# Optimization experiments

Hardware: AMD Instinct MI355X
Metric: run time of the kernel (lower is better)

Reference implementation:

```python
import jax, jax.numpy as jnp
import numpy as np

N_NODES = 50000
N_EDGES = 600000
N_DISCRETE = 70
NH = N_DISCRETE - 6          # 64
EMB = 128                    # n_embedding
D = NH + EMB                 # 192, resdnn/cross input dim
RES_HID = 512                # l_hidden entries
N_RES = 2                    # len(l_hidden)
N_CROSS = 2
PRED_HID = (2 * NH + 512) // 2  # 320
NEG_SLOPE = 0.01


def setup_inputs() -> dict:
    key = jax.random.key(0)
    ks = jax.random.split(key, 24)
    def w(k, shape, fan_in):
        return (jax.random.normal(k, shape, jnp.float32) / np.sqrt(fan_in)).astype(jnp.float32)
    inp = {
        "discrete_x": jax.random.randint(ks[0], (N_NODES, N_DISCRETE), 0, 100, jnp.int64),
        "edge_index": jax.random.randint(ks[1], (2, N_EDGES), 0, N_NODES, jnp.int64),
        # graph embedding linear + 2 GCN layers
        "w_g0": w(ks[2], (NH, EMB), NH), "b_g0": jnp.zeros((EMB,), jnp.float32),
        "w_gcn1": w(ks[3], (EMB, EMB), EMB), "b_gcn1": jnp.zeros((EMB,), jnp.float32),
        "w_gcn2": w(ks[4], (EMB, EMB), EMB), "b_gcn2": jnp.zeros((EMB,), jnp.float32),
        # ResDNN: N_RES dim-preserving residual bottleneck blocks D->RES_HID->D
        "res_w1": w(ks[5], (N_RES, D, RES_HID), D), "res_b1": jnp.zeros((N_RES, RES_HID), jnp.float32),
        "res_w2": w(ks[6], (N_RES, RES_HID, D), RES_HID), "res_b2": jnp.zeros((N_RES, D), jnp.float32),
        # CrossNet: N_CROSS layers
        "cross_w": w(ks[7], (N_CROSS, D), D), "cross_b": jnp.zeros((N_CROSS, D), jnp.float32),
        # Prediction MLP: 2D -> PRED_HID -> 1, sigmoid
        "p_w1": w(ks[8], (2 * D, PRED_HID), 2 * D), "p_b1": jnp.zeros((PRED_HID,), jnp.float32),
        "p_w2": w(ks[9], (PRED_HID, 1), PRED_HID), "p_b2": jnp.zeros((1,), jnp.float32),
    }
    return inp


def _leaky(x):
    return jax.nn.leaky_relu(x, NEG_SLOPE)


def _gcn_conv(x, W, b, row, col, n):
    # PyG GCNConv: linear, then sym-normalized aggregation over A + I, then bias
    h = x @ W
    deg = jax.ops.segment_sum(jnp.ones(row.shape, x.dtype), col, num_segments=n) + 1.0
    dinv = jax.lax.rsqrt(deg)
    norm = dinv[row] * dinv[col]            # [E]
    msg = h[row] * norm[:, None]            # [E, EMB]  (largest intermediate)
    agg = jax.ops.segment_sum(msg, col, num_segments=n)
    agg = agg + h * (dinv * dinv)[:, None]  # self-loop contribution
    return agg + b


def reference(discrete_x, edge_index, w_g0, b_g0, w_gcn1, b_gcn1, w_gcn2, b_gcn2,
              res_w1, res_b1, res_w2, res_b2, cross_w, cross_b,
              p_w1, p_b1, p_w2, p_b2):
    n = discrete_x.shape[0]
    row, col = edge_index[0], edge_index[1]
    # DiscreteFeatureEmbeddingLayer: map n_discrete_features int cols -> nh float dims
    x_d = discrete_x[:, :NH].astype(jnp.float32)
    # graph branch
    x_g = _leaky(x_d @ w_g0 + b_g0)
    x_g = _leaky(_gcn_conv(x_g, w_gcn1, b_gcn1, row, col, n))
    x_g = _leaky(_gcn_conv(x_g, w_gcn2, b_gcn2, row, col, n))
    x = jnp.concatenate([x_d, x_g], axis=-1)  # [N, D]
    # ResDNN: residual bottleneck blocks
    x_deep = x
    for i in range(N_RES):
        h = _leaky(x_deep @ res_w1[i] + res_b1[i])
        x_deep = _leaky(x_deep + h @ res_w2[i] + res_b2[i])
    # CrossNet (DCN): x_{l+1} = x0 * (x_l . w_l) + b_l + x_l
    x0 = x
    x_cross = x
    for i in range(N_CROSS):
        xw = x_cross @ cross_w[i]            # [N]
        x_cross = x0 * xw[:, None] + cross_b[i] + x_cross
    z = jnp.concatenate([x_deep, x_cross], axis=-1)  # [N, 2D]
    h = _leaky(z @ p_w1 + p_b1)
    y = jax.nn.sigmoid(h @ p_w2 + p_b2)
    return y.squeeze(-1)
```

## Files before the change

kernel.cpp:

```cpp
#include <hip/hip_runtime.h>
#include <math.h>

constexpr int NCOLS   = 70;
constexpr int NH      = 64;
constexpr int EMB     = 128;
constexpr int DD      = 192;
constexpr int RES_HID = 512;
constexpr int PRED_HID= 320;

typedef _Float16 f16x8 __attribute__((ext_vector_type(8)));
typedef float    f32x4 __attribute__((ext_vector_type(4)));
#define MFMA16F(a,b,c) __builtin_amdgcn_mfma_f32_16x16x32_f16((a),(b),(c),0,0,0)

constexpr float LO_SCALE   = 4096.0f;
constexpr float LO_DESCALE = 1.0f/4096.0f;
constexpr float Z_SCALE    = 0.0625f;
constexpr float Z_DESCALE  = 16.0f;

__device__ __forceinline__ float leaky(float x){ return x > 0.f ? x : 0.01f*x; }

__global__ void k_hist(const int* __restrict__ col, int* __restrict__ cnt, int E){
  int e = blockIdx.x*256 + threadIdx.x;
  if (e < E) atomicAdd(&cnt[col[e]], 1);
}
__global__ void k_scanA(const int* __restrict__ cnt, int* __restrict__ bsum, int n){
  __shared__ int s;
  if (threadIdx.x == 0) s = 0;
  __syncthreads();
  int i = blockIdx.x*256 + threadIdx.x;
  int v = (i < n) ? cnt[i] : 0;
  #pragma unroll
  for (int o=32;o;o>>=1) v += __shfl_xor(v, o, 64);
  if ((threadIdx.x & 63) == 0) atomicAdd(&s, v);
  __syncthreads();
  if (threadIdx.x == 0) bsum[blockIdx.x] = s;
}
__global__ void k_scanB(int* bsum, int nb){
  __shared__ int s[256];
  __shared__ int carry;
  if (threadIdx.x == 0) carry = 0;
  __syncthreads();
  for (int start = 0; start < nb; start += 256){
    int i = start + threadIdx.x;
    int v = (i < nb) ? bsum[i] : 0;
    s[threadIdx.x] = v; __syncthreads();
    for (int o=1;o<256;o<<=1){
      int t = (threadIdx.x >= o) ? s[threadIdx.x-o] : 0;
      __syncthreads();
      s[threadIdx.x] += t; __syncthreads();
    }
    if (i < nb) bsum[i] = carry + s[threadIdx.x] - v;
    __syncthreads();
    if (threadIdx.x == 255) carry += s[255];
    __syncthreads();
  }
}
__global__ void k_scanC(const int* __restrict__ cnt, const int* __restrict__ bsum,
                        int* __restrict__ base, int* __restrict__ cursor,
                        float* __restrict__ dinv, int n, int E){
  __shared__ int s[256];
  int i = blockIdx.x*256 + threadIdx.x;
  int v = (i < n) ? cnt[i] : 0;
  s[threadIdx.x] = v; __syncthreads();
  for (int o=1;o<256;o<<=1){
    int t = (threadIdx.x >= o) ? s[threadIdx.x-o] : 0;
    __syncthreads();
    s[threadIdx.x] += t; __syncthreads();
  }
  if (i < n){
    int b = bsum[blockIdx.x] + s[threadIdx.x] - v;
    base[i] = b; cursor[i] = b;
    dinv[i] = rsqrtf((float)(v + 1));
  }
  if (i == n-1) base[n] = E;
}
__global__ void k_fill(const int* __restrict__ row, const int* __restrict__ col,
                       const float* __restrict__ dinv, int* __restrict__ cursor,
                       int2* __restrict__ ebin, int E){
  int e = blockIdx.x*256 + threadIdx.x;
  if (e < E){
    int r = row[e], c = col[e];
    int slot = atomicAdd(&cursor[c], 1);
    ebin[slot] = make_int2(r, __float_as_int(dinv[r]));
  }
}

__device__ __forceinline__ void pack_one(const float* __restrict__ W,
                                         _Float16* __restrict__ Wh, _Float16* __restrict__ Wl,
                                         int K, int N, int local){
  int k = local / N, nn = local - k*N;
  float v = W[local];
  _Float16 h = (_Float16)v;
  float lo = (v - (float)h)*LO_SCALE;
  int kc = k >> 5, r = k & 31;
  int lane = (nn & 15) | ((r >> 3) << 4);
  int j = r & 7;
  size_t dst = ((size_t)((nn >> 4)*(K >> 5) + kc) << 9) + lane*8 + j;
  Wh[dst] = h;
  Wl[dst] = (_Float16)lo;
}
__global__ void k_wprep_all(const float* res_w1, const float* res_w2, const float* p_w1,
                            const float* w_g0, const float* w_gcn1, const float* w_gcn2,
                            _Float16* wt1h, _Float16* wt1l, _Float16* wt2h, _Float16* wt2l,
                            _Float16* wph, _Float16* wpl, _Float16* wg0h, _Float16* wg0l,
                            _Float16* wg1h, _Float16* wg1l, _Float16* wg2h, _Float16* wg2l)
{
  int idx = blockIdx.x*256 + threadIdx.x;
  constexpr int SZ = DD*RES_HID;
  constexpr int PZ = 2*DD*PRED_HID;
  if (idx < SZ)                 pack_one(res_w1,           wt1h,      wt1l,      DD, RES_HID, idx);
  else if (idx < 2*SZ)          pack_one(res_w1 + SZ,      wt1h + SZ, wt1l + SZ, DD, RES_HID, idx - SZ);
  else if (idx < 3*SZ)          pack_one(res_w2,           wt2h,      wt2l,      RES_HID, DD, idx - 2*SZ);
  else if (idx < 4*SZ)          pack_one(res_w2 + SZ,      wt2h + SZ, wt2l + SZ, RES_HID, DD, idx - 3*SZ);
  else if (idx < 4*SZ + PZ)     pack_one(p_w1,             wph,       wpl,       2*DD, PRED_HID, idx - 4*SZ);
  else if (idx < 4*SZ + PZ + NH*EMB)
                                pack_one(w_g0,             wg0h,      wg0l,      NH, EMB, idx - 4*SZ - PZ);
  else if (idx < 4*SZ + PZ + NH*EMB + EMB*EMB)
                                pack_one(w_gcn1,           wg1h,      wg1l,      EMB, EMB, idx - 4*SZ - PZ - NH*EMB);
  else if (idx < 4*SZ + PZ + NH*EMB + 2*EMB*EMB)
                                pack_one(w_gcn2,           wg2h,      wg2l,      EMB, EMB, idx - 4*SZ - PZ - NH*EMB - EMB*EMB);
}

__global__ void k_embed(const int* __restrict__ dx, float* __restrict__ A, int n){
  int idx = blockIdx.x*256 + threadIdx.x;
  if (idx < n*NH){
    int i = idx >> 6, j = idx & 63;
    A[(size_t)i*DD + j] = (float)dx[(size_t)i*NCOLS + j];
  }
}

template<int KC>
__global__ __launch_bounds__(256,3)
void k_lin_mfma2(const float* __restrict__ X, int ldx,
                 const _Float16* __restrict__ Wh, const _Float16* __restrict__ Wl,
                 const float* __restrict__ bias,
                 float* __restrict__ out, int ldo, int ooff, int n, int act)
{
  constexpr int K  = KC*32;
  constexpr int KS = K + 4;
  __shared__ __align__(16) _Float16 xh[32*KS];
  __shared__ __align__(16) _Float16 xl[32*KS];
  int i0 = blockIdx.x*32;
  for (int idx = threadIdx.x; idx < 32*K; idx += 256){
    int t = idx / K, k = idx - t*K;
    int i = i0 + t;
    float v = (i < n) ? X[(size_t)i*ldx + k] : 0.f;
    _Float16 h = (_Float16)v;
    xh[t*KS + k] = h;
    xl[t*KS + k] = (_Float16)((v - (float)h)*LO_SCALE);
  }
  __syncthreads();
  int wv = threadIdx.x >> 6, ln = threadIdx.x & 63;
  int cn = ln & 15, kg = ln >> 4;
  f16x8 A0h[KC], A0l[KC], A1h[KC], A1l[KC];
  #pragma unroll
  for (int kc=0;kc<KC;kc++){
    int k0 = kc*32 + kg*8;
    A0h[kc] = *(const f16x8*)&xh[cn*KS + k0];
    A0l[kc] = *(const f16x8*)&xl[cn*KS + k0];
    A1h[kc] = *(const f16x8*)&xh[(16+cn)*KS + k0];
    A1l[kc] = *(const f16x8*)&xl[(16+cn)*KS + k0];
  }
  #pragma unroll
  for (int t=0;t<2;t++){
    int nt = wv*2 + t, n0 = nt*16;
    const _Float16* wbh = Wh + (((size_t)nt*KC) << 9) + ln*8;
    const _Float16* wbl = Wl + (((size_t)nt*KC) << 9) + ln*8;
    f32x4 acc0={0.f,0.f,0.f,0.f}, accL0={0.f,0.f,0.f,0.f};
    f32x4 acc1={0.f,0.f,0.f,0.f}, accL1={0.f,0.f,0.f,0.f};
    #pragma unroll
    for (int kc=0;kc<KC;kc++){
      f16x8 bh = *(const f16x8*)(wbh + ((size_t)kc<<9));
      f16x8 bl = *(const f16x8*)(wbl + ((size_t)kc<<9));
      acc0  = MFMA16F(A0h[kc], bh, acc0);
      accL0 = MFMA16F(A0l[kc], bh, accL0);
      accL0 = MFMA16F(A0h[kc], bl, accL0);
      acc1  = MFMA16F(A1h[kc], bh, acc1);
      accL1 = MFMA16F(A1l[kc], bh, accL1);
      accL1 = MFMA16F(A1h[kc], bl, accL1);
    }
    float bb = bias ? bias[n0 + cn] : 0.f;
    #pragma unroll
    for (int r=0;r<4;r++){
      int ia = i0 + kg*4 + r, ib = ia + 16;
      float v0 = acc0[r] + accL0[r]*LO_DESCALE + bb;
      float v1 = acc1[r] + accL1[r]*LO_DESCALE + bb;
      if (act){ v0 = leaky(v0); v1 = leaky(v1); }
      if (ia < n) out[(size_t)ia*ldo + ooff + n0 + cn] = v0;
      if (ib < n) out[(size_t)ib*ldo + ooff + n0 + cn] = v1;
    }
  }
}

__global__ void k_gather(const float* __restrict__ h, const float* __restrict__ dinv,
                         const int* __restrict__ base, const int2* __restrict__ ebin,
                         const float* __restrict__ bias, float* __restrict__ out,
                         int ldo, int ooff, int n)
{
  int node = blockIdx.x*4 + (threadIdx.x >> 6);
  int lane = threadIdx.x & 63;
  if (node >= n) return;
  int half = lane >> 5, l32 = lane & 31;
  int b0 = base[node], b1 = base[node+1];
  float dc = dinv[node];
  float4 acc = {0.f,0.f,0.f,0.f};
  for (int e = b0 + half; e < b1; e += 2){
    int2 ee = ebin[e];
    float4 hv = ((const float4*)(h + (size_t)ee.x*EMB))[l32];
    float dd = __int_as_float(ee.y);
    acc.x = fmaf(hv.x, dd, acc.x);
    acc.y = fmaf(hv.y, dd, acc.y);
    acc.z = fmaf(hv.z, dd, acc.z);
    acc.w = fmaf(hv.w, dd, acc.w);
  }
  acc.x += __shfl_xor(acc.x, 32, 64);
  acc.y += __shfl_xor(acc.y, 32, 64);
  acc.z += __shfl_xor(acc.z, 32, 64);
  acc.w += __shfl_xor(acc.w, 32, 64);
  float4 hc = ((const float4*)(h + (size_t)node*EMB))[l32];
  float4 bv = ((const float4*)bias)[l32];
  float4 res;
  res.x = leaky((acc.x + hc.x*dc)*dc + bv.x);
  res.y = leaky((acc.y + hc.y*dc)*dc + bv.y);
  res.z = leaky((acc.z + hc.z*dc)*dc + bv.z);
  res.w = leaky((acc.w + hc.w*dc)*dc + bv.w);
  if (half == 0)
    *(float4*)(out + (size_t)node*ldo + ooff + 4*l32) = res;
}

constexpr int XS = 196;
constexpr int HS = 516;

__global__ __launch_bounds__(256,2)
void k_resblock_mfma(const float* __restrict__ X,
                     const _Float16* __restrict__ W1h, const _Float16* __restrict__ W1l,
                     const float* __restrict__ b1,
                     const _Float16* __restrict__ W2h, const _Float16* __restrict__ W2l,
                     const float* __restrict__ b2,
                     float* __restrict__ out, int n)
{
  __shared__ __align__(16) _Float16 xh[32*XS];
  __shared__ __align__(16) _Float16 xl[32*XS];
  __shared__ __align__(16) _Float16 hh[32*HS];
  int i0 = blockIdx.x*32;
  for (int idx = threadIdx.x; idx < 32*DD; idx += 256){
    int t = idx / DD, k = idx - t*DD;
    int i = i0 + t;
    float v = (i < n) ? X[(size_t)i*DD + k] : 0.f;
    _Float16 h = (_Float16)v;
    xh[t*XS + k] = h;
    xl[t*XS + k] = (_Float16)((v - (float)h)*LO_SCALE);
  }
  __syncthreads();
  int wv = threadIdx.x >> 6, ln = threadIdx.x & 63;
  int cn = ln & 15, kg = ln >> 4;

  {
    f16x8 A0h[6], A0l[6], A1h[6], A1l[6];
    #pragma unroll
    for (int kc=0;kc<6;kc++){
      int k0 = kc*32 + kg*8;
      A0h[kc] = *(const f16x8*)&xh[cn*XS + k0];
      A0l[kc] = *(const f16x8*)&xl[cn*XS + k0];
      A1h[kc] = *(const f16x8*)&xh[(16+cn)*XS + k0];
      A1l[kc] = *(const f16x8*)&xl[(16+cn)*XS + k0];
    }
    float bias1[8];
    #pragma unroll
    for (int ct=0;ct<8;ct++) bias1[ct] = b1[(wv*8+ct)*16 + cn];
    const _Float16* pbh = W1h + ((size_t)(wv*8)*6 << 9) + ln*8;
    const _Float16* pbl = W1l + ((size_t)(wv*8)*6 << 9) + ln*8;
    f16x8 Bh[6], Bl[6];
    #pragma unroll
    for (int kc=0;kc<6;kc++){
      Bh[kc] = *(const f16x8*)(pbh + ((size_t)kc<<9));
      Bl[kc] = *(const f16x8*)(pbl + ((size_t)kc<<9));
    }
    #pragma unroll 1
    for (int ct = 0; ct < 8; ct++){
      f16x8 Bh2[6], Bl2[6];
      if (ct < 7){
        const _Float16* nh = pbh + ((size_t)((ct+1)*6) << 9);
        const _Float16* nl = pbl + ((size_t)((ct+1)*6) << 9);
        #pragma unroll
        for (int kc=0;kc<6;kc++){
          Bh2[kc] = *(const f16x8*)(nh + ((size_t)kc<<9));
          Bl2[kc] = *(const f16x8*)(nl + ((size_t)kc<<9));
        }
      }
      f32x4 acc0={0.f,0.f,0.f,0.f}, accL0={0.f,0.f,0.f,0.f};
      f32x4 acc1={0.f,0.f,0.f,0.f}, accL1={0.f,0.f,0.f,0.f};
      #pragma unroll
      for (int kc=0;kc<6;kc++){
        acc0  = MFMA16F(A0h[kc], Bh[kc], acc0);
        accL0 = MFMA16F(A0l[kc], Bh[kc], accL0);
        accL0 = MFMA16F(A0h[kc], Bl[kc], accL0);
        acc1  = MFMA16F(A1h[kc], Bh[kc], acc1);
        accL1 = MFMA16F(A1l[kc], Bh[kc], accL1);
        accL1 = MFMA16F(A1h[kc], Bl[kc], accL1);
      }
      int n0 = (wv*8+ct)*16;
      float bb = bias1[ct];
      #pragma unroll
      for (int r=0;r<4;r++){
        hh[(kg*4+r)*HS + n0 + cn]    = (_Float16)leaky(acc0[r] + accL0[r]*LO_DESCALE + bb);
        hh[(16+kg*4+r)*HS + n0 + cn] = (_Float16)leaky(acc1[r] + accL1[r]*LO_DESCALE + bb);
      }
      #pragma unroll
      for (int kc=0;kc<6;kc++){ Bh[kc]=Bh2[kc]; Bl[kc]=Bl2[kc]; }
    }
  }
  __syncthreads();

  {
    f32x4 acc[3][2], accL[3][2];
    #pragma unroll
    for (int c=0;c<3;c++){
      #pragma unroll
      for (int g=0;g<2;g++){
        acc[c][g]  = (f32x4){0.f,0.f,0.f,0.f};
        accL[c][g] = (f32x4){0.f,0.f,0.f,0.f};
      }
    }
    f16x8 B2h[3], B2l[3];
    #pragma unroll
    for (int c=0;c<3;c++){
      size_t off = ((size_t)((wv*3+c)*16) << 9) + ln*8;
      B2h[c] = *(const f16x8*)(W2h + off);
      B2l[c] = *(const f16x8*)(W2l + off);
    }
    #pragma unroll 1
    for (int kc=0;kc<16;kc++){
      f16x8 N2h[3], N2l[3];
      if (kc < 15){
        #pragma unroll
        for (int c=0;c<3;c++){
          size_t off = ((size_t)((wv*3+c)*16 + kc + 1) << 9) + ln*8;
          N2h[c] = *(const f16x8*)(W2h + off);
          N2l[c] = *(const f16x8*)(W2l + off);
        }
      }
      int k0 = kc*32 + kg*8;
      f16x8 a0 = *(const f16x8*)&hh[cn*HS + k0];
      f16x8 a1 = *(const f16x8*)&hh[(16+cn)*HS + k0];
      #pragma unroll
      for (int c=0;c<3;c++){
        acc[c][0]  = MFMA16F(a0, B2h[c], acc[c][0]);
        accL[c][0] = MFMA16F(a0, B2l[c], accL[c][0]);
        acc[c][1]  = MFMA16F(a1, B2h[c], acc[c][1]);
        accL[c][1] = MFMA16F(a1, B2l[c], accL[c][1]);
      }
      #pragma unroll
      for (int c=0;c<3;c++){ B2h[c]=N2h[c]; B2l[c]=N2l[c]; }
    }
    #pragma unroll
    for (int c=0;c<3;c++){
      int n0 = (wv*3+c)*16;
      float bb = b2[n0 + cn];
      #pragma unroll
      for (int r=0;r<4;r++){
        int m0 = kg*4 + r, m1 = 16 + kg*4 + r;
        float res0 = (float)xh[m0*XS + n0 + cn] + (float)xl[m0*XS + n0 + cn]*LO_DESCALE;
        float res1 = (float)xh[m1*XS + n0 + cn] + (float)xl[m1*XS + n0 + cn]*LO_DESCALE;
        int ia = i0 + m0, ib = i0 + m1;
        if (ia < n) out[(size_t)ia*DD + n0 + cn] = leaky(res0 + acc[c][0][r] + accL[c][0][r]*LO_DESCALE + bb);
        if (ib < n) out[(size_t)ib*DD + n0 + cn] = leaky(res1 + acc[c][1][r] + accL[c][1][r]*LO_DESCALE + bb);
      }
    }
  }
}

constexpr int ZS = 392;

__global__ __launch_bounds__(256,3)
void k_pred_mfma(const float* __restrict__ deep, const float* __restrict__ X0,
                 const float* __restrict__ cw, const float* __restrict__ cb,
                 const _Float16* __restrict__ Wh, const _Float16* __restrict__ Wl,
                 const float* __restrict__ b1,
                 const float* __restrict__ w2, const float* __restrict__ b2,
                 float* __restrict__ y, int n)
{
  __shared__ __align__(16) _Float16 zh[32*ZS];
  __shared__ __align__(16) _Float16 zl[32*ZS];
  __shared__ float sred[4][32];
  int i0 = blockIdx.x*32;
  for (int idx = threadIdx.x; idx < 32*DD; idx += 256){
    int t = idx / DD, k = idx - t*DD;
    int i = i0 + t;
    float v = (i < n) ? deep[(size_t)i*DD + k] : 0.f;
    v *= Z_SCALE;
    _Float16 h = (_Float16)v;
    zh[t*ZS + k] = h;
    zl[t*ZS + k] = (_Float16)((v - (float)h)*LO_SCALE);
  }
  int wv = threadIdx.x >> 6, ln = threadIdx.x & 63;
  for (int m = 0; m < 8; m++){
    int t = wv*8 + m;
    int node = i0 + t;
    float v0[3], xc[3];
    if (node < n){
      const float* xr = X0 + (size_t)node*DD;
      #pragma unroll
      for (int q=0;q<3;q++){ v0[q] = xr[ln + 64*q]; xc[q] = v0[q]; }
      #pragma unroll
      for (int l=0;l<2;l++){
        float p = 0.f;
        #pragma unroll
        for (int q=0;q<3;q++) p += xc[q]*cw[l*DD + ln + 64*q];
        #pragma unroll
        for (int off=32; off>0; off>>=1) p += __shfl_xor(p, off, 64);
        #pragma unroll
        for (int q=0;q<3;q++) xc[q] = v0[q]*p + cb[l*DD + ln + 64*q] + xc[q];
      }
    } else {
      #pragma unroll
      for (int q=0;q<3;q++) xc[q] = 0.f;
    }
    #pragma unroll
    for (int q=0;q<3;q++){
      float v = xc[q]*Z_SCALE;
      _Float16 h = (_Float16)v;
      zh[t*ZS + DD + ln + 64*q] = h;
      zl[t*ZS + DD + ln + 64*q] = (_Float16)((v - (float)h)*LO_SCALE);
    }
  }
  __syncthreads();
  int cn = ln & 15, kg = ln >> 4;
  float vs0[4] = {0.f,0.f,0.f,0.f};
  float vs1[4] = {0.f,0.f,0.f,0.f};
  #pragma unroll 1
  for (int ct = 0; ct < 5; ct++){
    int nt = wv*5 + ct;
    int n0 = nt*16;
    f32x4 acc0 = {0.f,0.f,0.f,0.f}, accL0 = {0.f,0.f,0.f,0.f};
    f32x4 acc1 = {0.f,0.f,0.f,0.f}, accL1 = {0.f,0.f,0.f,0.f};
    const _Float16* wbh = Wh + ((size_t)nt*12 << 9) + ln*8;
    const _Float16* wbl = Wl + ((size_t)nt*12 << 9) + ln*8;
    #pragma unroll 4
    for (int kc = 0; kc < 12; kc++){
      f16x8 bh = *(const f16x8*)(wbh + (kc << 9));
      f16x8 bl = *(const f16x8*)(wbl + (kc << 9));
      int k0 = kc*32 + kg*8;
      f16x8 a0h = *(const f16x8*)&zh[cn*ZS + k0];
      f16x8 a0l = *(const f16x8*)&zl[cn*ZS + k0];
      f16x8 a1h = *(const f16x8*)&zh[(16+cn)*ZS + k0];
      f16x8 a1l = *(const f16x8*)&zl[(16+cn)*ZS + k0];
      acc0  = MFMA16F(a0h, bh, acc0);
      accL0 = MFMA16F(a0l, bh, accL0);
      accL0 = MFMA16F(a0h, bl, accL0);
      acc1  = MFMA16F(a1h, bh, acc1);
      accL1 = MFMA16F(a1l, bh, accL1);
      accL1 = MFMA16F(a1h, bl, accL1);
    }
    float bb = b1[n0 + cn];
    float ww = w2[n0 + cn];
    #pragma unroll
    for (int r=0;r<4;r++){
      float v0 = (acc0[r] + accL0[r]*LO_DESCALE)*Z_DESCALE + bb;
      float v1 = (acc1[r] + accL1[r]*LO_DESCALE)*Z_DESCALE + bb;
      vs0[r] += leaky(v0)*ww;
      vs1[r] += leaky(v1)*ww;
    }
  }
  #pragma unroll
  for (int r=0;r<4;r++){
    #pragma unroll
    for (int off=1; off<16; off<<=1){
      vs0[r] += __shfl_xor(vs0[r], off, 64);
      vs1[r] += __shfl_xor(vs1[r], off, 64);
    }
  }
  if (cn == 0){
    #pragma unroll
    for (int r=0;r<4;r++){
      sred[wv][kg*4 + r]      = vs0[r];
      sred[wv][16 + kg*4 + r] = vs1[r];
    }
  }
  __syncthreads();
  if (threadIdx.x < 32){
    int m = threadIdx.x;
    float s = sred[0][m] + sred[1][m] + sred[2][m] + sred[3][m] + b2[0];
    int i = i0 + m;
    if (i < n) y[i] = 1.f/(1.f + expf(-s));
  }
}

extern "C" void kernel_launch(void* const* d_in, const int* in_sizes, int n_in,
                              void* d_out, int out_size, void* d_ws, size_t ws_size,
                              hipStream_t stream)
{
  const int*   dx      = (const int*)d_in[0];
  const int*   ei      = (const int*)d_in[1];
  const float* w_g0    = (const float*)d_in[2];
  const float* b_g0    = (const float*)d_in[3];
  const float* w_gcn1  = (const float*)d_in[4];
  const float* b_gcn1  = (const float*)d_in[5];
  const float* w_gcn2  = (const float*)d_in[6];
  const float* b_gcn2  = (const float*)d_in[7];
  const float* res_w1  = (const float*)d_in[8];
  const float* res_b1  = (const float*)d_in[9];
  const float* res_w2  = (const float*)d_in[10];
  const float* res_b2  = (const float*)d_in[11];
  const float* cross_w = (const float*)d_in[12];
  const float* cross_b = (const float*)d_in[13];
  const float* p_w1    = (const float*)d_in[14];
  const float* p_b1    = (const float*)d_in[15];
  const float* p_w2    = (const float*)d_in[16];
  const float* p_b2    = (const float*)d_in[17];
  float* y = (float*)d_out;

  int n = in_sizes[0] / NCOLS;
  int E = in_sizes[1] / 2;
  const int* row = ei;
  const int* col = ei + E;

  float* ws  = (float*)d_ws;
  float* A   = ws;
  float* B   = A  + (size_t)192*n;
  float* G   = B  + (size_t)192*n;
  float* E1  = G;
  float* E2v = G  + (size_t)128*n;
  float* dinv= G  + (size_t)256*n;
  int*  cnt    = (int*)(dinv + n);
  int*  base   = cnt + n;
  int*  cursor = base + n + 2;
  int*  bsum   = cursor + n;
  int2* ebin   = (int2*)((((uintptr_t)(bsum + 256)) + 15) & ~(uintptr_t)15);
  _Float16* wt1h = (_Float16*)((((uintptr_t)(ebin + E)) + 15) & ~(uintptr_t)15);
  _Float16* wt1l = wt1h + (size_t)2*RES_HID*DD;
  _Float16* wt2h = wt1l + (size_t)2*RES_HID*DD;
  _Float16* wt2l = wt2h + (size_t)2*RES_HID*DD;
  _Float16* wph  = wt2l + (size_t)2*RES_HID*DD;
  _Float16* wpl  = wph  + (size_t)PRED_HID*2*DD;
  _Float16* wg0h = wpl  + (size_t)PRED_HID*2*DD;
  _Float16* wg0l = wg0h + (size_t)NH*EMB;
  _Float16* wg1h = wg0l + (size_t)NH*EMB;
  _Float16* wg1l = wg1h + (size_t)EMB*EMB;
  _Float16* wg2h = wg1l + (size_t)EMB*EMB;
  _Float16* wg2l = wg2h + (size_t)EMB*EMB;

  dim3 blk(256);
  int nb = (n + 255)/256;

  {
    int total = 4*DD*RES_HID + 2*DD*PRED_HID + NH*EMB + 2*EMB*EMB;
    k_wprep_all<<<(total+255)/256, blk, 0, stream>>>(res_w1, res_w2, p_w1, w_g0, w_gcn1, w_gcn2,
                                                     wt1h, wt1l, wt2h, wt2l, wph, wpl,
                                                     wg0h, wg0l, wg1h, wg1l, wg2h, wg2l);
  }

  hipMemsetAsync(cnt, 0, (size_t)n*sizeof(int), stream);
  k_hist <<<(E+255)/256, blk, 0, stream>>>(col, cnt, E);
  k_scanA<<<nb, blk, 0, stream>>>(cnt, bsum, n);
  k_scanB<<<1, blk, 0, stream>>>(bsum, nb);
  k_scanC<<<nb, blk, 0, stream>>>(cnt, bsum, base, cursor, dinv, n, E);
  k_fill <<<(E+255)/256, blk, 0, stream>>>(row, col, dinv, cursor, ebin, E);

  int rbt = (n + 31)/32;
  k_embed<<<(n*NH+255)/256, blk, 0, stream>>>(dx, A, n);
  k_lin_mfma2<2><<<rbt, blk, 0, stream>>>(A, DD, wg0h, wg0l, b_g0, E1, EMB, 0, n, 1);
  k_lin_mfma2<4><<<rbt, blk, 0, stream>>>(E1, EMB, wg1h, wg1l, nullptr, E2v, EMB, 0, n, 0);
  k_gather  <<<(n+3)/4, blk, 0, stream>>>(E2v, dinv, base, ebin, b_gcn1, E1, EMB, 0, n);
  k_lin_mfma2<4><<<rbt, blk, 0, stream>>>(E1, EMB, wg2h, wg2l, nullptr, E2v, EMB, 0, n, 0);
  k_gather  <<<(n+3)/4, blk, 0, stream>>>(E2v, dinv, base, ebin, b_gcn2, A, DD, NH, n);
  k_resblock_mfma<<<rbt, blk, 0, stream>>>(A, wt1h, wt1l, res_b1,
                                           wt2h, wt2l, res_b2, B, n);
  k_resblock_mfma<<<rbt, blk, 0, stream>>>(B, wt1h + (size_t)DD*RES_HID, wt1l + (size_t)DD*RES_HID,
                                           res_b1 + RES_HID,
                                           wt2h + (size_t)DD*RES_HID, wt2l + (size_t)DD*RES_HID,
                                           res_b2 + DD, B, n);
  k_pred_mfma<<<rbt, blk, 0, stream>>>(B, A, cross_w, cross_b, wph, wpl, p_b1, p_w2, p_b2, y, n);
}
```

Measured before the change: 631.5 us.

## Alias resblock shared buffers and drop weight prefetch to raise occupancy

The residual block kernel now reuses one shared buffer for the fp16 input split and the hidden activations. The A fragments are held in registers and a barrier is placed before the hidden tile overwrites the input. The double-buffered weight prefetch registers are removed and the launch bound goes from 2 to 3 blocks per CU, aiming for more waves to hide latency. The residual is re-read in full fp32 from global memory instead of the split fp16 copy, which adds global reads and exposes weight-load latency that the prefetch used to hide.

```diff
diff --git a/kernel.cpp b/kernel.cpp
--- a/kernel.cpp
+++ b/kernel.cpp
@@ -231,7 +231,7 @@
 constexpr int XS = 196;
 constexpr int HS = 516;
 
-__global__ __launch_bounds__(256,2)
+__global__ __launch_bounds__(256,3)
 void k_resblock_mfma(const float* __restrict__ X,
                      const _Float16* __restrict__ W1h, const _Float16* __restrict__ W1l,
                      const float* __restrict__ b1,
@@ -239,9 +239,10 @@
                      const float* __restrict__ b2,
                      float* __restrict__ out, int n)
 {
-  __shared__ __align__(16) _Float16 xh[32*XS];
-  __shared__ __align__(16) _Float16 xl[32*XS];
-  __shared__ __align__(16) _Float16 hh[32*HS];
+  __shared__ __align__(16) _Float16 smem[32*HS];
+  _Float16* xh = smem;
+  _Float16* xl = smem + 32*XS;
+  _Float16* hh = smem;
   int i0 = blockIdx.x*32;
   for (int idx = threadIdx.x; idx < 32*DD; idx += 256){
     int t = idx / DD, k = idx - t*DD;
@@ -254,60 +255,40 @@
   __syncthreads();
   int wv = threadIdx.x >> 6, ln = threadIdx.x & 63;
   int cn = ln & 15, kg = ln >> 4;
-
-  {
-    f16x8 A0h[6], A0l[6], A1h[6], A1l[6];
+  f16x8 A0h[6], A0l[6], A1h[6], A1l[6];
+  #pragma unroll
+  for (int kc=0;kc<6;kc++){
+    int k0 = kc*32 + kg*8;
+    A0h[kc] = *(const f16x8*)&xh[cn*XS + k0];
+    A0l[kc] = *(const f16x8*)&xl[cn*XS + k0];
+    A1h[kc] = *(const f16x8*)&xh[(16+cn)*XS + k0];
+    A1l[kc] = *(const f16x8*)&xl[(16+cn)*XS + k0];
+  }
+  __syncthreads();
+
+  #pragma unroll 1
+  for (int ct = 0; ct < 8; ct++){
+    int nt = wv*8 + ct, n0 = nt*16;
+    const _Float16* wbh = W1h + (((size_t)nt*6) << 9) + ln*8;
+    const _Float16* wbl = W1l + (((size_t)nt*6) << 9) + ln*8;
+    f32x4 acc0={0.f,0.f,0.f,0.f}, accL0={0.f,0.f,0.f,0.f};
+    f32x4 acc1={0.f,0.f,0.f,0.f}, accL1={0.f,0.f,0.f,0.f};
     #pragma unroll
     for (int kc=0;kc<6;kc++){
-      int k0 = kc*32 + kg*8;
-      A0h[kc] = *(const f16x8*)&xh[cn*XS + k0];
-      A0l[kc] = *(const f16x8*)&xl[cn*XS + k0];
-      A1h[kc] = *(const f16x8*)&xh[(16+cn)*XS + k0];
-      A1l[kc] = *(const f16x8*)&xl[(16+cn)*XS + k0];
-    }
-    float bias1[8];
-    #pragma unroll
-    for (int ct=0;ct<8;ct++) bias1[ct] = b1[(wv*8+ct)*16 + cn];
-    const _Float16* pbh = W1h + ((size_t)(wv*8)*6 << 9) + ln*8;
-    const _Float16* pbl = W1l + ((size_t)(wv*8)*6 << 9) + ln*8;
-    f16x8 Bh[6], Bl[6];
-    #pragma unroll
-    for (int kc=0;kc<6;kc++){
-      Bh[kc] = *(const f16x8*)(pbh + ((size_t)kc<<9));
-      Bl[kc] = *(const f16x8*)(pbl + ((size_t)kc<<9));
-    }
-    #pragma unroll 1
-    for (int ct = 0; ct < 8; ct++){
-      f16x8 Bh2[6], Bl2[6];
-      if (ct < 7){
-        const _Float16* nh = pbh + ((size_t)((ct+1)*6) << 9);
-        const _Float16* nl = pbl + ((size_t)((ct+1)*6) << 9);
-        #pragma unroll
-        for (int kc=0;kc<6;kc++){
-          Bh2[kc] = *(const f16x8*)(nh + ((size_t)kc<<9));
-          Bl2[kc] = *(const f16x8*)(nl + ((size_t)kc<<9));
-        }
-      }
-      f32x4 acc0={0.f,0.f,0.f,0.f}, accL0={0.f,0.f,0.f,0.f};
-      f32x4 acc1={0.f,0.f,0.f,0.f}, accL1={0.f,0.f,0.f,0.f};
-      #pragma unroll
-      for (int kc=0;kc<6;kc++){
-        acc0  = MFMA16F(A0h[kc], Bh[kc], acc0);
-        accL0 = MFMA16F(A0l[kc], Bh[kc], accL0);
-        accL0 = MFMA16F(A0h[kc], Bl[kc], accL0);
-        acc1  = MFMA16F(A1h[kc], Bh[kc], acc1);
-        accL1 = MFMA16F(A1l[kc], Bh[kc], accL1);
-        accL1 = MFMA16F(A1h[kc], Bl[kc], accL1);
-      }
-      int n0 = (wv*8+ct)*16;
-      float bb = bias1[ct];
-      #pragma unroll
-      for (int r=0;r<4;r++){
-        hh[(kg*4+r)*HS + n0 + cn]    = (_Float16)leaky(acc0[r] + accL0[r]*LO_DESCALE + bb);
-        hh[(16+kg*4+r)*HS + n0 + cn] = (_Float16)leaky(acc1[r] + accL1[r]*LO_DESCALE + bb);
-      }
-      #pragma unroll
-      for (int kc=0;kc<6;kc++){ Bh[kc]=Bh2[kc]; Bl[kc]=Bl2[kc]; }
+      f16x8 bh = *(const f16x8*)(wbh + ((size_t)kc<<9));
+      f16x8 bl = *(const f16x8*)(wbl + ((size_t)kc<<9));
+      acc0  = MFMA16F(A0h[kc], bh, acc0);
+      accL0 = MFMA16F(A0l[kc], bh, accL0);
+      accL0 = MFMA16F(A0h[kc], bl, accL0);
+      acc1  = MFMA16F(A1h[kc], bh, acc1);
+      accL1 = MFMA16F(A1l[kc], bh, accL1);
+      accL1 = MFMA16F(A1h[kc], bl, accL1);
+    }
+    float bb = b1[n0 + cn];
+    #pragma unroll
+    for (int r=0;r<4;r++){
+      hh[(kg*4+r)*HS + n0 + cn]    = (_Float16)leaky(acc0[r] + accL0[r]*LO_DESCALE + bb);
+      hh[(16+kg*4+r)*HS + n0 + cn] = (_Float16)leaky(acc1[r] + accL1[r]*LO_DESCALE + bb);
     }
   }
   __syncthreads();
@@ -322,23 +303,14 @@
         accL[c][g] = (f32x4){0.f,0.f,0.f,0.f};
       }
     }
-    f16x8 B2h[3], B2l[3];
-    #pragma unroll
-    for (int c=0;c<3;c++){
-      size_t off = ((size_t)((wv*3+c)*16) << 9) + ln*8;
-      B2h[c] = *(const f16x8*)(W2h + off);
-      B2l[c] = *(const f16x8*)(W2l + off);
-    }
     #pragma unroll 1
     for (int kc=0;kc<16;kc++){
-      f16x8 N2h[3], N2l[3];
-      if (kc < 15){
-        #pragma unroll
-        for (int c=0;c<3;c++){
-          size_t off = ((size_t)((wv*3+c)*16 + kc + 1) << 9) + ln*8;
-          N2h[c] = *(const f16x8*)(W2h + off);
-          N2l[c] = *(const f16x8*)(W2l + off);
-        }
+      f16x8 B2h[3], B2l[3];
+      #pragma unroll
+      for (int c=0;c<3;c++){
+        size_t off = ((size_t)((wv*3+c)*16 + kc) << 9) + ln*8;
+        B2h[c] = *(const f16x8*)(W2h + off);
+        B2l[c] = *(const f16x8*)(W2l + off);
       }
       int k0 = kc*32 + kg*8;
       f16x8 a0 = *(const f16x8*)&hh[cn*HS + k0];
@@ -350,8 +322,6 @@
         acc[c][1]  = MFMA16F(a1, B2h[c], acc[c][1]);
         accL[c][1] = MFMA16F(a1, B2l[c], accL[c][1]);
       }
-      #pragma unroll
-      for (int c=0;c<3;c++){ B2h[c]=N2h[c]; B2l[c]=N2l[c]; }
     }
     #pragma unroll
     for (int c=0;c<3;c++){
@@ -360,11 +330,15 @@
       #pragma unroll
       for (int r=0;r<4;r++){
         int m0 = kg*4 + r, m1 = 16 + kg*4 + r;
-        float res0 = (float)xh[m0*XS + n0 + cn] + (float)xl[m0*XS + n0 + cn]*LO_DESCALE;
-        float res1 = (float)xh[m1*XS + n0 + cn] + (float)xl[m1*XS + n0 + cn]*LO_DESCALE;
         int ia = i0 + m0, ib = i0 + m1;
-        if (ia < n) out[(size_t)ia*DD + n0 + cn] = leaky(res0 + acc[c][0][r] + accL[c][0][r]*LO_DESCALE + bb);
-        if (ib < n) out[(size_t)ib*DD + n0 + cn] = leaky(res1 + acc[c][1][r] + accL[c][1][r]*LO_DESCALE + bb);
+        if (ia < n){
+          float res = X[(size_t)ia*DD + n0 + cn];
+          out[(size_t)ia*DD + n0 + cn] = leaky(res + acc[c][0][r] + accL[c][0][r]*LO_DESCALE + bb);
+        }
+        if (ib < n){
+          float res = X[(size_t)ib*DD + n0 + cn];
+          out[(size_t)ib*DD + n0 + cn] = leaky(res + acc[c][1][r] + accL[c][1][r]*LO_DESCALE + bb);
+        }
       }
     }
   }
```

New measurement: 662.3 us. 1.05x slower.
